# Performance work log

Measured on AMD Instinct MI355X. Metric: run time of the kernel, lower is better.

The kernel has to match this reference:

```python
import jax, jax.numpy as jnp
import numpy as np

N_NODES = 100000
N_EDGES = 1250000
D_IN, D_HID, D_OUT = 64, 128, 64


def _seg_mean(msg, dst, n):
    # mean aggregation over incoming neighbors (PyG SAGEConv aggr='mean')
    s = jax.ops.segment_sum(msg, dst, num_segments=n)
    cnt = jax.ops.segment_sum(jnp.ones((msg.shape[0], 1), msg.dtype), dst, num_segments=n)
    return s / jnp.maximum(cnt, 1.0)


def setup_inputs() -> dict:
    key = jax.random.key(0)
    ks = jax.random.split(key, 8)
    x = jax.random.normal(ks[0], (N_NODES, D_IN), dtype=jnp.float32)
    edge_index = jax.random.randint(ks[1], (2, N_EDGES), 0, N_NODES, dtype=jnp.int32)
    # SAGEConv params: lin_l (on aggregated neighbors, with bias), lin_r (on root, no bias)
    s1 = 1.0 / np.sqrt(D_IN)
    s2 = 1.0 / np.sqrt(D_HID)
    W1_l = jax.random.normal(ks[2], (D_IN, D_HID), dtype=jnp.float32) * s1
    W1_r = jax.random.normal(ks[3], (D_IN, D_HID), dtype=jnp.float32) * s1
    b1 = jnp.zeros((D_HID,), dtype=jnp.float32)
    W2_l = jax.random.normal(ks[4], (D_HID, D_OUT), dtype=jnp.float32) * s2
    W2_r = jax.random.normal(ks[5], (D_HID, D_OUT), dtype=jnp.float32) * s2
    b2 = jnp.zeros((D_OUT,), dtype=jnp.float32)
    return {"x": x, "edge_index": edge_index, "W1_l": W1_l, "b1": b1, "W1_r": W1_r,
            "W2_l": W2_l, "b2": b2, "W2_r": W2_r}


def reference(x, edge_index, W1_l, b1, W1_r, W2_l, b2, W2_r):
    n = x.shape[0]
    src, dst = edge_index[0], edge_index[1]
    # layer 1: SAGEConv = lin_l(mean_{j in N(i)} x_j) + lin_r(x_i)
    agg1 = _seg_mean(x[src], dst, n)                      # [N, D_IN]
    h = agg1 @ W1_l + b1 + x @ W1_r                       # [N, D_HID]
    h = jax.nn.relu(h)                                    # dropout is identity in eval
    # layer 2
    agg2 = _seg_mean(h[src], dst, n)                      # [N, D_HID]
    out = agg2 @ W2_l + b2 + h @ W2_r                     # [N, D_OUT]
    return out
```

## Files before the change

kernel.cpp:

```cpp
#include <hip/hip_runtime.h>

#define NN 100000
#define NE 1250000

#define NBLK1 320
#define CHUNK 3907
#define NBUK  196
#define CAP   8192

#define SCALE_X 23.0f
#define SCALE_P 24.0f

typedef __attribute__((ext_vector_type(8))) short short8;
typedef __attribute__((ext_vector_type(4))) float f32x4;

static constexpr size_t I_BH    = 0;
static constexpr size_t I_BT    = 62720;
static constexpr size_t I_BB    = 62976;
static constexpr size_t I_OFFS  = 63232;
static constexpr size_t I_PAIRS = 163236;
static constexpr size_t I_SSRC  = 1413236;
static constexpr size_t B_UBASE = 10652944;
static constexpr size_t B_XB    = 0;
static constexpr size_t B_AGG   = 12800000;
static constexpr size_t B_WF1   = 25600000;
static constexpr size_t B_WF2   = 25632768;
static constexpr size_t B_XQ    = 25665536;
static constexpr size_t B_PQ    = 32065536;

__device__ __forceinline__ float bf2f(unsigned int u16) {
    unsigned int v = u16 << 16;
    return __builtin_bit_cast(float, v);
}
__device__ __forceinline__ unsigned int f2bf(float f) {
    unsigned int u = __builtin_bit_cast(unsigned int, f);
    return (u + 0x7fffu + ((u >> 16) & 1u)) >> 16;
}
__device__ __forceinline__ int f2i8(float f, float scale) {
    float c = fminf(fmaxf(f * scale, -127.f), 127.f);
    return (int)rintf(c);
}

__global__ __launch_bounds__(256) void conv_x(const float* __restrict__ x,
                                              unsigned short* __restrict__ xb,
                                              char* __restrict__ xq)
{
    int t = blockIdx.x * 256 + threadIdx.x;
    int n = t >> 3, c8 = (t & 7) * 8;
    const float* xp = x + (size_t)n * 64 + c8;
    float4 v0 = *(const float4*)(xp);
    float4 v1 = *(const float4*)(xp + 4);
    uint4 o;
    o.x = f2bf(v0.x) | (f2bf(v0.y) << 16);
    o.y = f2bf(v0.z) | (f2bf(v0.w) << 16);
    o.z = f2bf(v1.x) | (f2bf(v1.y) << 16);
    o.w = f2bf(v1.z) | (f2bf(v1.w) << 16);
    *(uint4*)(xb + (size_t)n * 64 + c8) = o;
    uint2 q;
    q.x = (f2i8(v0.x, SCALE_X) & 0xff) | ((f2i8(v0.y, SCALE_X) & 0xff) << 8) |
          ((f2i8(v0.z, SCALE_X) & 0xff) << 16) | ((unsigned)(f2i8(v0.w, SCALE_X) & 0xff) << 24);
    q.y = (f2i8(v1.x, SCALE_X) & 0xff) | ((f2i8(v1.y, SCALE_X) & 0xff) << 8) |
          ((f2i8(v1.z, SCALE_X) & 0xff) << 16) | ((unsigned)(f2i8(v1.w, SCALE_X) & 0xff) << 24);
    *(uint2*)(xq + (size_t)n * 64 + c8) = q;
}

__global__ __launch_bounds__(256) void prep_w(
    const float* __restrict__ W1l, const float* __restrict__ W1r,
    const float* __restrict__ W2l, const float* __restrict__ W2r,
    unsigned short* __restrict__ Wf1, unsigned short* __restrict__ Wf2)
{
    int i = blockIdx.x * 256 + threadIdx.x;
    if (i >= 16384) return;
    int e    = i & 7;
    int ch   = i >> 3;
    int lrow = ch & 15;
    int lk   = (ch >> 4) & 3;
    int kk   = (ch >> 6) & 3;
    int c    = ch >> 8;
    int j = c * 16 + lrow;
    int k = kk * 32 + lk * 8 + e;
    float w1 = (k < 64) ? W1l[(size_t)k * 128 + j] : W1r[(size_t)(k - 64) * 128 + j];
    Wf1[i] = (unsigned short)f2bf(w1);
    float w2 = (j < 64) ? W2l[(size_t)k * 64 + j] : W2r[(size_t)k * 64 + (j - 64)];
    Wf2[i] = (unsigned short)f2bf(w2);
}

__global__ __launch_bounds__(512) void p0_hist(const int* __restrict__ dstv,
                                               int* __restrict__ blockHist)
{
    __shared__ int hist[NBUK];
    const int t = threadIdx.x, b = blockIdx.x;
    for (int i = t; i < NBUK; i += 512) hist[i] = 0;
    __syncthreads();
    const int start = b * CHUNK;
    const int end   = min(start + CHUNK, NE);
    for (int e = start + t; e < end; e += 512)
        atomicAdd(&hist[dstv[e] >> 9], 1);
    __syncthreads();
    for (int i = t; i < NBUK; i += 512)
        blockHist[(size_t)i * NBLK1 + b] = hist[i];
}

__global__ __launch_bounds__(512) void p_scanA(int* __restrict__ blockHist,
                                               int* __restrict__ bucketTot)
{
    __shared__ int s[512];
    const int b = blockIdx.x, t = threadIdx.x;
    int v = (t < NBLK1) ? blockHist[(size_t)b * NBLK1 + t] : 0;
    s[t] = v;
    __syncthreads();
    for (int d = 1; d < 512; d <<= 1) {
        int x = (t >= d) ? s[t - d] : 0;
        __syncthreads();
        s[t] += x;
        __syncthreads();
    }
    if (t < NBLK1) blockHist[(size_t)b * NBLK1 + t] = s[t] - v;
    if (t == NBLK1 - 1) bucketTot[b] = s[t];
}

__global__ __launch_bounds__(256) void p_scanB(const int* __restrict__ bucketTot,
                                               int* __restrict__ bucketBase,
                                               int* __restrict__ offs)
{
    __shared__ int s[256];
    const int t = threadIdx.x;
    int v = (t < NBUK) ? bucketTot[t] : 0;
    s[t] = v;
    __syncthreads();
    for (int d = 1; d < 256; d <<= 1) {
        int x = (t >= d) ? s[t - d] : 0;
        __syncthreads();
        s[t] += x;
        __syncthreads();
    }
    if (t < NBUK) bucketBase[t] = s[t] - v;
    if (t == 0) { bucketBase[NBUK] = NE; offs[NN] = NE; }
}

__global__ __launch_bounds__(512) void p1_scatter(
    const int* __restrict__ srcv, const int* __restrict__ dstv,
    const int* __restrict__ blockHist, const int* __restrict__ bucketBase,
    int* __restrict__ pairs)
{
    __shared__ int cur[NBUK];
    const int t = threadIdx.x, b = blockIdx.x;
    for (int i = t; i < NBUK; i += 512)
        cur[i] = bucketBase[i] + blockHist[(size_t)i * NBLK1 + b];
    __syncthreads();
    const int start = b * CHUNK;
    const int end   = min(start + CHUNK, NE);
    for (int e = start + t; e < end; e += 512) {
        int d = dstv[e], s = srcv[e];
        int pos = atomicAdd(&cur[d >> 9], 1);
        pairs[pos] = s | ((d & 511) << 17);
    }
}

__global__ __launch_bounds__(1024) void p2_sort(
    const int* __restrict__ pairs, const int* __restrict__ bucketBase,
    int* __restrict__ offs, int* __restrict__ ssrc)
{
    __shared__ int buf[CAP];
    __shared__ int hist[512];
    const int b = blockIdx.x, t = threadIdx.x;
    const int base = bucketBase[b];
    const int m    = bucketBase[b + 1] - base;
    const bool fits = (m <= CAP);

    if (t < 512) hist[t] = 0;
    __syncthreads();
    for (int i = t; i < m; i += 1024) {
        int v = pairs[base + i];
        if (fits) buf[i] = v;
        atomicAdd(&hist[v >> 17], 1);
    }
    __syncthreads();

    int ov = (t < 512) ? hist[t] : 0;
    __syncthreads();
    for (int d = 1; d < 512; d <<= 1) {
        int x = 0;
        if (t < 512 && t >= d) x = hist[t - d];
        __syncthreads();
        if (t < 512) hist[t] += x;
        __syncthreads();
    }
    int excl = 0;
    if (t < 512) excl = hist[t] - ov;
    __syncthreads();
    if (t < 512) {
        hist[t] = excl;
        int n = b * 512 + t;
        if (n < NN) offs[n] = base + excl;
    }
    __syncthreads();
    for (int i = t; i < m; i += 1024) {
        int v = fits ? buf[i] : pairs[base + i];
        int pos = atomicAdd(&hist[v >> 17], 1);
        ssrc[base + pos] = v & 0x1FFFF;
    }
}

template <int FUSE>
__global__ __launch_bounds__(256) void sage_gather(
    const int* __restrict__ offs, const int* __restrict__ ssrc,
    const char* __restrict__ feat,
    const float* __restrict__ b2,
    unsigned short* __restrict__ aggb, float* __restrict__ out)
{
    const int t = blockIdx.x * 256 + threadIdx.x;
    const int n   = t >> 5;
    const int l   = t & 31;
    const int par = l >> 3;
    const int ch  = l & 7;
    const int e0 = offs[n], e1 = offs[n + 1];

    int ai[8];
    #pragma unroll
    for (int j = 0; j < 8; ++j) ai[j] = 0;

    int e = e0 + par;
    for (; e + 4 < e1; e += 8) {
        int s0 = ssrc[e], s1 = ssrc[e + 4];
        uint2 u = *(const uint2*)(feat + (size_t)s0 * 64 + ch * 8);
        uint2 v = *(const uint2*)(feat + (size_t)s1 * 64 + ch * 8);
        ai[0] += (int)(signed char)(u.x)       + (int)(signed char)(v.x);
        ai[1] += (int)(signed char)(u.x >> 8)  + (int)(signed char)(v.x >> 8);
        ai[2] += (int)(signed char)(u.x >> 16) + (int)(signed char)(v.x >> 16);
        ai[3] += (int)(signed char)(u.x >> 24) + (int)(signed char)(v.x >> 24);
        ai[4] += (int)(signed char)(u.y)       + (int)(signed char)(v.y);
        ai[5] += (int)(signed char)(u.y >> 8)  + (int)(signed char)(v.y >> 8);
        ai[6] += (int)(signed char)(u.y >> 16) + (int)(signed char)(v.y >> 16);
        ai[7] += (int)(signed char)(u.y >> 24) + (int)(signed char)(v.y >> 24);
    }
    if (e < e1) {
        int s0 = ssrc[e];
        uint2 u = *(const uint2*)(feat + (size_t)s0 * 64 + ch * 8);
        ai[0] += (int)(signed char)(u.x);
        ai[1] += (int)(signed char)(u.x >> 8);
        ai[2] += (int)(signed char)(u.x >> 16);
        ai[3] += (int)(signed char)(u.x >> 24);
        ai[4] += (int)(signed char)(u.y);
        ai[5] += (int)(signed char)(u.y >> 8);
        ai[6] += (int)(signed char)(u.y >> 16);
        ai[7] += (int)(signed char)(u.y >> 24);
    }
    #pragma unroll
    for (int j = 0; j < 8; ++j) ai[j] += __shfl_xor(ai[j], 8);
    #pragma unroll
    for (int j = 0; j < 8; ++j) ai[j] += __shfl_xor(ai[j], 16);
    if (par) return;

    const int dg = e1 - e0;
    const float mul = 1.0f / ((float)(dg > 0 ? dg : 1) *
                              (FUSE == 0 ? SCALE_X : SCALE_P));
    float acc[8];
    #pragma unroll
    for (int j = 0; j < 8; ++j) acc[j] = (float)ai[j] * mul;

    if (FUSE == 0) {
        uint4 o;
        o.x = f2bf(acc[0]) | (f2bf(acc[1]) << 16);
        o.y = f2bf(acc[2]) | (f2bf(acc[3]) << 16);
        o.z = f2bf(acc[4]) | (f2bf(acc[5]) << 16);
        o.w = f2bf(acc[6]) | (f2bf(acc[7]) << 16);
        *(uint4*)(aggb + (size_t)n * 64 + ch * 8) = o;
    } else {
        float* o = out + (size_t)n * 64 + ch * 8;
        float4 q0 = *(const float4*)(o);
        float4 q1 = *(const float4*)(o + 4);
        float4 c0 = *(const float4*)(b2 + ch * 8);
        float4 c1 = *(const float4*)(b2 + ch * 8 + 4);
        *(float4*)(o)     = make_float4(acc[0] + q0.x + c0.x, acc[1] + q0.y + c0.y,
                                        acc[2] + q0.z + c0.z, acc[3] + q0.w + c0.w);
        *(float4*)(o + 4) = make_float4(acc[4] + q1.x + c1.x, acc[5] + q1.y + c1.y,
                                        acc[6] + q1.z + c1.z, acc[7] + q1.w + c1.w);
    }
}

__global__ __launch_bounds__(256) void sage_fused(
    const unsigned short* __restrict__ agg, const unsigned short* __restrict__ xb,
    const unsigned short* __restrict__ Wf1, const unsigned short* __restrict__ Wf2,
    const float* __restrict__ b1,
    char* __restrict__ pq, float* __restrict__ outq)
{
    __shared__ __align__(16) unsigned short sW1[16384];
    __shared__ __align__(16) unsigned short sW2[16384];
    __shared__ __align__(16) unsigned short sh[4][2048];

    const int tid  = threadIdx.x;
    const int lane = tid & 63;
    const int wid  = tid >> 6;
    const int lrow = lane & 15;
    const int lk   = lane >> 4;

    {
        const uint4* g1 = (const uint4*)Wf1;
        const uint4* g2 = (const uint4*)Wf2;
        uint4* s1 = (uint4*)sW1;
        uint4* s2 = (uint4*)sW2;
        #pragma unroll
        for (int i = 0; i < 8; ++i) {
            int idx = tid + i * 256;
            s1[idx] = g1[idx];
            s2[idx] = g2[idx];
        }
    }
    __syncthreads();

    const int rbase = blockIdx.x * 64 + wid * 16;
    int arow = rbase + lrow;
    if (arow >= NN) arow = NN - 1;

    short8 a1[4];
    #pragma unroll
    for (int kk = 0; kk < 4; ++kk) {
        int k0 = kk * 32 + lk * 8;
        const unsigned short* ap = (k0 < 64) ? (agg + (size_t)arow * 64 + k0)
                                             : (xb  + (size_t)arow * 64 + (k0 - 64));
        a1[kk] = *(const short8*)ap;
    }

    const int fragoff = (lk * 16 + lrow) * 8;

    f32x4 acc1[8];
    #pragma unroll
    for (int c = 0; c < 8; ++c) {
        acc1[c] = (f32x4){0.f, 0.f, 0.f, 0.f};
        #pragma unroll
        for (int kk = 0; kk < 4; ++kk) {
            short8 b = *(const short8*)(sW1 + fragoff + c * 2048 + kk * 512);
            acc1[c] = __builtin_amdgcn_mfma_f32_16x16x32_bf16(a1[kk], b, acc1[c], 0, 0, 0);
        }
    }

    unsigned short* myh = &sh[wid][0];
    #pragma unroll
    for (int c = 0; c < 8; ++c) {
        float bv = b1[c * 16 + lrow];
        int chbase = ((2 * c + (lrow >> 3)) * 16 + lk * 4) * 8 + (lrow & 7);
        #pragma unroll
        for (int ri = 0; ri < 4; ++ri) {
            float v = fmaxf(acc1[c][ri] + bv, 0.f);
            myh[chbase + ri * 8] = (unsigned short)f2bf(v);
        }
    }

    short8 a2[4];
    #pragma unroll
    for (int kk = 0; kk < 4; ++kk)
        a2[kk] = *(const short8*)(myh + fragoff + kk * 512);

    f32x4 acc2[8];
    #pragma unroll
    for (int c = 0; c < 8; ++c) {
        acc2[c] = (f32x4){0.f, 0.f, 0.f, 0.f};
        #pragma unroll
        for (int kk = 0; kk < 4; ++kk) {
            short8 b = *(const short8*)(sW2 + fragoff + c * 2048 + kk * 512);
            acc2[c] = __builtin_amdgcn_mfma_f32_16x16x32_bf16(a2[kk], b, acc2[c], 0, 0, 0);
        }
    }

    #pragma unroll
    for (int c = 0; c < 8; ++c) {
        int col = c * 16 + lrow;
        #pragma unroll
        for (int ri = 0; ri < 4; ++ri) {
            int row = rbase + lk * 4 + ri;
            if (row >= NN) continue;
            if (col < 64) pq[(size_t)row * 64 + col] = (char)f2i8(acc2[c][ri], SCALE_P);
            else          outq[(size_t)row * 64 + (col - 64)] = acc2[c][ri];
        }
    }
}

extern "C" void kernel_launch(void* const* d_in, const int* in_sizes, int n_in,
                              void* d_out, int out_size, void* d_ws, size_t ws_size,
                              hipStream_t stream)
{
    const float* x    = (const float*)d_in[0];
    const int*   ei   = (const int*)d_in[1];
    const float* W1_l = (const float*)d_in[2];
    const float* b1   = (const float*)d_in[3];
    const float* W1_r = (const float*)d_in[4];
    const float* W2_l = (const float*)d_in[5];
    const float* b2   = (const float*)d_in[6];
    const float* W2_r = (const float*)d_in[7];

    float* out = (float*)d_out;
    int*   wi  = (int*)d_ws;
    char*  ub  = (char*)d_ws + B_UBASE;

    const int* srcv = ei;
    const int* dstv = ei + NE;

    int* blockHist  = wi + I_BH;
    int* bucketTot  = wi + I_BT;
    int* bucketBase = wi + I_BB;
    int* offs       = wi + I_OFFS;
    int* pairs      = wi + I_PAIRS;
    int* ssrc       = wi + I_SSRC;
    unsigned short* xb  = (unsigned short*)(ub + B_XB);
    unsigned short* agg = (unsigned short*)(ub + B_AGG);
    unsigned short* Wf1 = (unsigned short*)(ub + B_WF1);
    unsigned short* Wf2 = (unsigned short*)(ub + B_WF2);
    char* xq = ub + B_XQ;
    char* pq = ub + B_PQ;

    conv_x <<<(NN * 8) / 256, 256, 0, stream>>>(x, xb, xq);
    prep_w <<<64, 256, 0, stream>>>(W1_l, W1_r, W2_l, W2_r, Wf1, Wf2);

    p0_hist   <<<NBLK1, 512, 0, stream>>>(dstv, blockHist);
    p_scanA   <<<NBUK, 512, 0, stream>>>(blockHist, bucketTot);
    p_scanB   <<<1, 256, 0, stream>>>(bucketTot, bucketBase, offs);
    p1_scatter<<<NBLK1, 512, 0, stream>>>(srcv, dstv, blockHist, bucketBase, pairs);
    p2_sort   <<<NBUK, 1024, 0, stream>>>(pairs, bucketBase, offs, ssrc);

    sage_gather<0><<<(NN * 32) / 256, 256, 0, stream>>>(offs, ssrc, xq, nullptr, agg, nullptr);

    sage_fused<<<(NN + 63) / 64, 256, 0, stream>>>(agg, xb, Wf1, Wf2, b1, pq, out);

    sage_gather<1><<<(NN * 32) / 256, 256, 0, stream>>>(offs, ssrc, pq, b2, nullptr, out);
}
```

Before: 127.8 us.

## Fuse layer-1 neighbor gather into the fused MLP kernel via shared memory

Moves the layer-1 mean aggregation into the sage_fused kernel: each block gathers int8 neighbor features for its 64 nodes, converts to bf16 in LDS, and feeds them directly into the MFMA matmuls. This removes a kernel launch and the global write/read of the bf16 aggregate buffer. It trades away per-node gather parallelism (4 threads per node instead of 32) and serializes gather before MFMA work in each block. Workspace layout and offs padding are adjusted accordingly.

```diff
diff --git a/kernel.cpp b/kernel.cpp
--- a/kernel.cpp
+++ b/kernel.cpp
@@ -18,15 +18,14 @@
 static constexpr size_t I_BT    = 62720;
 static constexpr size_t I_BB    = 62976;
 static constexpr size_t I_OFFS  = 63232;
-static constexpr size_t I_PAIRS = 163236;
-static constexpr size_t I_SSRC  = 1413236;
-static constexpr size_t B_UBASE = 10652944;
+static constexpr size_t I_PAIRS = 163344;
+static constexpr size_t I_SSRC  = 1413344;
+static constexpr size_t B_UBASE = 10653376;
 static constexpr size_t B_XB    = 0;
-static constexpr size_t B_AGG   = 12800000;
-static constexpr size_t B_WF1   = 25600000;
-static constexpr size_t B_WF2   = 25632768;
-static constexpr size_t B_XQ    = 25665536;
-static constexpr size_t B_PQ    = 32065536;
+static constexpr size_t B_WF1   = 12800000;
+static constexpr size_t B_WF2   = 12832768;
+static constexpr size_t B_XQ    = 12865536;
+static constexpr size_t B_PQ    = 19265536;
 
 __device__ __forceinline__ float bf2f(unsigned int u16) {
     unsigned int v = u16 << 16;
@@ -135,7 +134,8 @@
         __syncthreads();
     }
     if (t < NBUK) bucketBase[t] = s[t] - v;
-    if (t == 0) { bucketBase[NBUK] = NE; offs[NN] = NE; }
+    if (t == 0) bucketBase[NBUK] = NE;
+    if (t < 100) offs[NN + t] = NE;
 }
 
 __global__ __launch_bounds__(512) void p1_scatter(
@@ -202,12 +202,175 @@
     }
 }
 
-template <int FUSE>
-__global__ __launch_bounds__(256) void sage_gather(
+__global__ __launch_bounds__(256) void sage_fused(
     const int* __restrict__ offs, const int* __restrict__ ssrc,
-    const char* __restrict__ feat,
+    const char* __restrict__ xq,
+    const unsigned short* __restrict__ xb,
+    const unsigned short* __restrict__ Wf1, const unsigned short* __restrict__ Wf2,
+    const float* __restrict__ b1,
+    char* __restrict__ pq, float* __restrict__ outq)
+{
+    __shared__ __align__(16) unsigned short sW1[16384];
+    __shared__ __align__(16) unsigned short sW2[16384];
+    __shared__ __align__(16) unsigned short uni[8192];
+
+    unsigned short* sAgg = uni;
+    int* s_off = (int*)((char*)uni + 9216);
+
+    const int tid = threadIdx.x;
+
+    {
+        const uint4* g1 = (const uint4*)Wf1;
+        const uint4* g2 = (const uint4*)Wf2;
+        uint4* s1 = (uint4*)sW1;
+        uint4* s2 = (uint4*)sW2;
+        #pragma unroll
+        for (int i = 0; i < 8; ++i) {
+            int idx = tid + i * 256;
+            s1[idx] = g1[idx];
+            s2[idx] = g2[idx];
+        }
+    }
+    const int n0 = blockIdx.x * 64;
+    if (tid < 65) s_off[tid] = offs[n0 + tid];
+    __syncthreads();
+
+    {
+        const int r  = tid >> 2;
+        const int q2 = tid & 3;
+        const int ge0 = s_off[r], ge1 = s_off[r + 1];
+        int ai[16];
+        #pragma unroll
+        for (int j = 0; j < 16; ++j) ai[j] = 0;
+        int e = ge0;
+        for (; e + 1 < ge1; e += 2) {
+            int s0 = ssrc[e], s1 = ssrc[e + 1];
+            uint4 u = *(const uint4*)(xq + (size_t)s0 * 64 + q2 * 16);
+            uint4 v = *(const uint4*)(xq + (size_t)s1 * 64 + q2 * 16);
+            ai[0] += (int)(signed char)(u.x)       + (int)(signed char)(v.x);
+            ai[1] += (int)(signed char)(u.x >> 8)  + (int)(signed char)(v.x >> 8);
+            ai[2] += (int)(signed char)(u.x >> 16) + (int)(signed char)(v.x >> 16);
+            ai[3] += (int)(signed char)(u.x >> 24) + (int)(signed char)(v.x >> 24);
+            ai[4] += (int)(signed char)(u.y)       + (int)(signed char)(v.y);
+            ai[5] += (int)(signed char)(u.y >> 8)  + (int)(signed char)(v.y >> 8);
+            ai[6] += (int)(signed char)(u.y >> 16) + (int)(signed char)(v.y >> 16);
+            ai[7] += (int)(signed char)(u.y >> 24) + (int)(signed char)(v.y >> 24);
+            ai[8]  += (int)(signed char)(u.z)       + (int)(signed char)(v.z);
+            ai[9]  += (int)(signed char)(u.z >> 8)  + (int)(signed char)(v.z >> 8);
+            ai[10] += (int)(signed char)(u.z >> 16) + (int)(signed char)(v.z >> 16);
+            ai[11] += (int)(signed char)(u.z >> 24) + (int)(signed char)(v.z >> 24);
+            ai[12] += (int)(signed char)(u.w)       + (int)(signed char)(v.w);
+            ai[13] += (int)(signed char)(u.w >> 8)  + (int)(signed char)(v.w >> 8);
+            ai[14] += (int)(signed char)(u.w >> 16) + (int)(signed char)(v.w >> 16);
+            ai[15] += (int)(signed char)(u.w >> 24) + (int)(signed char)(v.w >> 24);
+        }
+        if (e < ge1) {
+            int s0 = ssrc[e];
+            uint4 u = *(const uint4*)(xq + (size_t)s0 * 64 + q2 * 16);
+            ai[0] += (int)(signed char)(u.x);
+            ai[1] += (int)(signed char)(u.x >> 8);
+            ai[2] += (int)(signed char)(u.x >> 16);
+            ai[3] += (int)(signed char)(u.x >> 24);
+            ai[4] += (int)(signed char)(u.y);
+            ai[5] += (int)(signed char)(u.y >> 8);
+            ai[6] += (int)(signed char)(u.y >> 16);
+            ai[7] += (int)(signed char)(u.y >> 24);
+            ai[8]  += (int)(signed char)(u.z);
+            ai[9]  += (int)(signed char)(u.z >> 8);
+            ai[10] += (int)(signed char)(u.z >> 16);
+            ai[11] += (int)(signed char)(u.z >> 24);
+            ai[12] += (int)(signed char)(u.w);
+            ai[13] += (int)(signed char)(u.w >> 8);
+            ai[14] += (int)(signed char)(u.w >> 16);
+            ai[15] += (int)(signed char)(u.w >> 24);
+        }
+        const int dg = ge1 - ge0;
+        const float mul = 1.0f / ((float)(dg > 0 ? dg : 1) * SCALE_X);
+        unsigned int o[8];
+        #pragma unroll
+        for (int j = 0; j < 8; ++j)
+            o[j] = f2bf((float)ai[2 * j] * mul) |
+                   (f2bf((float)ai[2 * j + 1] * mul) << 16);
+        *(uint4*)(sAgg + r * 72 + q2 * 16)     = make_uint4(o[0], o[1], o[2], o[3]);
+        *(uint4*)(sAgg + r * 72 + q2 * 16 + 8) = make_uint4(o[4], o[5], o[6], o[7]);
+    }
+    __syncthreads();
+
+    const int lane = tid & 63;
+    const int wid  = tid >> 6;
+    const int lrow = lane & 15;
+    const int lk   = lane >> 4;
+    const int rbase = n0 + wid * 16;
+    const int rloc  = wid * 16 + lrow;
+    int arow = rbase + lrow;
+    if (arow >= NN) arow = NN - 1;
+
+    short8 a1[4];
+    a1[0] = *(const short8*)(sAgg + rloc * 72 + lk * 8);
+    a1[1] = *(const short8*)(sAgg + rloc * 72 + 32 + lk * 8);
+    a1[2] = *(const short8*)(xb + (size_t)arow * 64 + lk * 8);
+    a1[3] = *(const short8*)(xb + (size_t)arow * 64 + 32 + lk * 8);
+    __syncthreads();
+
+    const int fragoff = (lk * 16 + lrow) * 8;
+
+    f32x4 acc1[8];
+    #pragma unroll
+    for (int c = 0; c < 8; ++c) {
+        acc1[c] = (f32x4){0.f, 0.f, 0.f, 0.f};
+        #pragma unroll
+        for (int kk = 0; kk < 4; ++kk) {
+            short8 b = *(const short8*)(sW1 + fragoff + c * 2048 + kk * 512);
+            acc1[c] = __builtin_amdgcn_mfma_f32_16x16x32_bf16(a1[kk], b, acc1[c], 0, 0, 0);
+        }
+    }
+
+    unsigned short* myh = uni + wid * 2048;
+    #pragma unroll
+    for (int c = 0; c < 8; ++c) {
+        float bv = b1[c * 16 + lrow];
+        int chbase = ((2 * c + (lrow >> 3)) * 16 + lk * 4) * 8 + (lrow & 7);
+        #pragma unroll
+        for (int ri = 0; ri < 4; ++ri) {
+            float v = fmaxf(acc1[c][ri] + bv, 0.f);
+            myh[chbase + ri * 8] = (unsigned short)f2bf(v);
+        }
+    }
+
+    short8 a2[4];
+    #pragma unroll
+    for (int kk = 0; kk < 4; ++kk)
+        a2[kk] = *(const short8*)(myh + fragoff + kk * 512);
+
+    f32x4 acc2[8];
+    #pragma unroll
+    for (int c = 0; c < 8; ++c) {
+        acc2[c] = (f32x4){0.f, 0.f, 0.f, 0.f};
+        #pragma unroll
+        for (int kk = 0; kk < 4; ++kk) {
+            short8 b = *(const short8*)(sW2 + fragoff + c * 2048 + kk * 512);
+            acc2[c] = __builtin_amdgcn_mfma_f32_16x16x32_bf16(a2[kk], b, acc2[c], 0, 0, 0);
+        }
+    }
+
+    #pragma unroll
+    for (int c = 0; c < 8; ++c) {
+        int col = c * 16 + lrow;
+        #pragma unroll
+        for (int ri = 0; ri < 4; ++ri) {
+            int row = rbase + lk * 4 + ri;
+            if (row >= NN) continue;
+            if (col < 64) pq[(size_t)row * 64 + col] = (char)f2i8(acc2[c][ri], SCALE_P);
+            else          outq[(size_t)row * 64 + (col - 64)] = acc2[c][ri];
+        }
+    }
+}
+
+__global__ __launch_bounds__(256) void sage_gather2(
+    const int* __restrict__ offs, const int* __restrict__ ssrc,
+    const char* __restrict__ pq,
     const float* __restrict__ b2,
-    unsigned short* __restrict__ aggb, float* __restrict__ out)
+    float* __restrict__ out)
 {
     const int t = blockIdx.x * 256 + threadIdx.x;
     const int n   = t >> 5;
@@ -223,8 +386,8 @@
     int e = e0 + par;
     for (; e + 4 < e1; e += 8) {
         int s0 = ssrc[e], s1 = ssrc[e + 4];
-        uint2 u = *(const uint2*)(feat + (size_t)s0 * 64 + ch * 8);
-        uint2 v = *(const uint2*)(feat + (size_t)s1 * 64 + ch * 8);
+        uint2 u = *(const uint2*)(pq + (size_t)s0 * 64 + ch * 8);
+        uint2 v = *(const uint2*)(pq + (size_t)s1 * 64 + ch * 8);
         ai[0] += (int)(signed char)(u.x)       + (int)(signed char)(v.x);
         ai[1] += (int)(signed char)(u.x >> 8)  + (int)(signed char)(v.x >> 8);
         ai[2] += (int)(signed char)(u.x >> 16) + (int)(signed char)(v.x >> 16);
@@ -236,7 +399,7 @@
     }
     if (e < e1) {
         int s0 = ssrc[e];
-        uint2 u = *(const uint2*)(feat + (size_t)s0 * 64 + ch * 8);
+        uint2 u = *(const uint2*)(pq + (size_t)s0 * 64 + ch * 8);
         ai[0] += (int)(signed char)(u.x);
         ai[1] += (int)(signed char)(u.x >> 8);
         ai[2] += (int)(signed char)(u.x >> 16);
@@ -253,127 +416,20 @@
     if (par) return;
 
     const int dg = e1 - e0;
-    const float mul = 1.0f / ((float)(dg > 0 ? dg : 1) *
-                              (FUSE == 0 ? SCALE_X : SCALE_P));
+    const float mul = 1.0f / ((float)(dg > 0 ? dg : 1) * SCALE_P);
     float acc[8];
     #pragma unroll
     for (int j = 0; j < 8; ++j) acc[j] = (float)ai[j] * mul;
 
-    if (FUSE == 0) {
-        uint4 o;
-        o.x = f2bf(acc[0]) | (f2bf(acc[1]) << 16);
-        o.y = f2bf(acc[2]) | (f2bf(acc[3]) << 16);
-        o.z = f2bf(acc[4]) | (f2bf(acc[5]) << 16);
-        o.w = f2bf(acc[6]) | (f2bf(acc[7]) << 16);
-        *(uint4*)(aggb + (size_t)n * 64 + ch * 8) = o;
-    } else {
-        float* o = out + (size_t)n * 64 + ch * 8;
-        float4 q0 = *(const float4*)(o);
-        float4 q1 = *(const float4*)(o + 4);
-        float4 c0 = *(const float4*)(b2 + ch * 8);
-        float4 c1 = *(const float4*)(b2 + ch * 8 + 4);
-        *(float4*)(o)     = make_float4(acc[0] + q0.x + c0.x, acc[1] + q0.y + c0.y,
-                                        acc[2] + q0.z + c0.z, acc[3] + q0.w + c0.w);
-        *(float4*)(o + 4) = make_float4(acc[4] + q1.x + c1.x, acc[5] + q1.y + c1.y,
-                                        acc[6] + q1.z + c1.z, acc[7] + q1.w + c1.w);
-    }
-}
-
-__global__ __launch_bounds__(256) void sage_fused(
-    const unsigned short* __restrict__ agg, const unsigned short* __restrict__ xb,
-    const unsigned short* __restrict__ Wf1, const unsigned short* __restrict__ Wf2,
-    const float* __restrict__ b1,
-    char* __restrict__ pq, float* __restrict__ outq)
-{
-    __shared__ __align__(16) unsigned short sW1[16384];
-    __shared__ __align__(16) unsigned short sW2[16384];
-    __shared__ __align__(16) unsigned short sh[4][2048];
-
-    const int tid  = threadIdx.x;
-    const int lane = tid & 63;
-    const int wid  = tid >> 6;
-    const int lrow = lane & 15;
-    const int lk   = lane >> 4;
-
-    {
-        const uint4* g1 = (const uint4*)Wf1;
-        const uint4* g2 = (const uint4*)Wf2;
-        uint4* s1 = (uint4*)sW1;
-        uint4* s2 = (uint4*)sW2;
-        #pragma unroll
-        for (int i = 0; i < 8; ++i) {
-            int idx = tid + i * 256;
-            s1[idx] = g1[idx];
-            s2[idx] = g2[idx];
-        }
-    }
-    __syncthreads();
-
-    const int rbase = blockIdx.x * 64 + wid * 16;
-    int arow = rbase + lrow;
-    if (arow >= NN) arow = NN - 1;
-
-    short8 a1[4];
-    #pragma unroll
-    for (int kk = 0; kk < 4; ++kk) {
-        int k0 = kk * 32 + lk * 8;
-        const unsigned short* ap = (k0 < 64) ? (agg + (size_t)arow * 64 + k0)
-                                             : (xb  + (size_t)arow * 64 + (k0 - 64));
-        a1[kk] = *(const short8*)ap;
-    }
-
-    const int fragoff = (lk * 16 + lrow) * 8;
-
-    f32x4 acc1[8];
-    #pragma unroll
-    for (int c = 0; c < 8; ++c) {
-        acc1[c] = (f32x4){0.f, 0.f, 0.f, 0.f};
-        #pragma unroll
-        for (int kk = 0; kk < 4; ++kk) {
-            short8 b = *(const short8*)(sW1 + fragoff + c * 2048 + kk * 512);
-            acc1[c] = __builtin_amdgcn_mfma_f32_16x16x32_bf16(a1[kk], b, acc1[c], 0, 0, 0);
-        }
-    }
-
-    unsigned short* myh = &sh[wid][0];
-    #pragma unroll
-    for (int c = 0; c < 8; ++c) {
-        float bv = b1[c * 16 + lrow];
-        int chbase = ((2 * c + (lrow >> 3)) * 16 + lk * 4) * 8 + (lrow & 7);
-        #pragma unroll
-        for (int ri = 0; ri < 4; ++ri) {
-            float v = fmaxf(acc1[c][ri] + bv, 0.f);
-            myh[chbase + ri * 8] = (unsigned short)f2bf(v);
-        }
-    }
-
-    short8 a2[4];
-    #pragma unroll
-    for (int kk = 0; kk < 4; ++kk)
-        a2[kk] = *(const short8*)(myh + fragoff + kk * 512);
-
-    f32x4 acc2[8];
-    #pragma unroll
-    for (int c = 0; c < 8; ++c) {
-        acc2[c] = (f32x4){0.f, 0.f, 0.f, 0.f};
-        #pragma unroll
-        for (int kk = 0; kk < 4; ++kk) {
-            short8 b = *(const short8*)(sW2 + fragoff + c * 2048 + kk * 512);
-            acc2[c] = __builtin_amdgcn_mfma_f32_16x16x32_bf16(a2[kk], b, acc2[c], 0, 0, 0);
-        }
-    }
-
-    #pragma unroll
-    for (int c = 0; c < 8; ++c) {
-        int col = c * 16 + lrow;
-        #pragma unroll
-        for (int ri = 0; ri < 4; ++ri) {
-            int row = rbase + lk * 4 + ri;
-            if (row >= NN) continue;
-            if (col < 64) pq[(size_t)row * 64 + col] = (char)f2i8(acc2[c][ri], SCALE_P);
-            else          outq[(size_t)row * 64 + (col - 64)] = acc2[c][ri];
-        }
-    }
+    float* o = out + (size_t)n * 64 + ch * 8;
+    float4 q0 = *(const float4*)(o);
+    float4 q1 = *(const float4*)(o + 4);
+    float4 c0 = *(const float4*)(b2 + ch * 8);
+    float4 c1 = *(const float4*)(b2 + ch * 8 + 4);
+    *(float4*)(o)     = make_float4(acc[0] + q0.x + c0.x, acc[1] + q0.y + c0.y,
+                                    acc[2] + q0.z + c0.z, acc[3] + q0.w + c0.w);
+    *(float4*)(o + 4) = make_float4(acc[4] + q1.x + c1.x, acc[5] + q1.y + c1.y,
+                                    acc[6] + q1.z + c1.z, acc[7] + q1.w + c1.w);
 }
 
 extern "C" void kernel_launch(void* const* d_in, const int* in_sizes, int n_in,
@@ -403,7 +459,6 @@
     int* pairs      = wi + I_PAIRS;
     int* ssrc       = wi + I_SSRC;
     unsigned short* xb  = (unsigned short*)(ub + B_XB);
-    unsigned short* agg = (unsigned short*)(ub + B_AGG);
     unsigned short* Wf1 = (unsigned short*)(ub + B_WF1);
     unsigned short* Wf2 = (unsigned short*)(ub + B_WF2);
     char* xq = ub + B_XQ;
@@ -418,9 +473,7 @@
     p1_scatter<<<NBLK1, 512, 0, stream>>>(srcv, dstv, blockHist, bucketBase, pairs);
     p2_sort   <<<NBUK, 1024, 0, stream>>>(pairs, bucketBase, offs, ssrc);
 
-    sage_gather<0><<<(NN * 32) / 256, 256, 0, stream>>>(offs, ssrc, xq, nullptr, agg, nullptr);
-
-    sage_fused<<<(NN + 63) / 64, 256, 0, stream>>>(agg, xb, Wf1, Wf2, b1, pq, out);
-
-    sage_gather<1><<<(NN * 32) / 256, 256, 0, stream>>>(offs, ssrc, pq, b2, nullptr, out);
-}
+    sage_fused<<<(NN + 63) / 64, 256, 0, stream>>>(offs, ssrc, xq, xb, Wf1, Wf2, b1, pq, out);
+
+    sage_gather2<<<(NN * 32) / 256, 256, 0, stream>>>(offs, ssrc, pq, b2, out);
+}
```

Result: no change. 129.9 us (+1.6%).
